# Kernel optimization log

Hardware: AMD Instinct MI355X
Metric: run time of the kernel (lower is better)

The kernel has to match this reference:

```python
import jax, jax.numpy as jnp
import numpy as np

N_NODES = 50000
N_EDGES = 800000
D_IN = 64
F1 = 64
F2 = 64
D_HID = 100


def setup_inputs() -> dict:
    key = jax.random.key(0)
    ks = jax.random.split(key, 12)
    x = jax.random.normal(ks[0], (N_NODES, D_IN), dtype=jnp.float32)
    edge_src = jax.random.randint(ks[1], (N_EDGES,), 0, N_NODES, dtype=jnp.int32)
    edge_dst = jax.random.randint(ks[2], (N_EDGES,), 0, N_NODES, dtype=jnp.int32)
    # stands in for pre-normalized GCN adjacency values (D^-1/2 (A+I) D^-1/2)
    edge_weight = jax.random.uniform(ks[3], (N_EDGES,), dtype=jnp.float32)
    def glorot(k, shape):
        lim = np.sqrt(6.0 / (shape[0] + shape[1]))
        return jax.random.uniform(k, shape, jnp.float32, -lim, lim)
    W1 = glorot(ks[4], (D_IN, F1))
    b1 = jnp.zeros((F1,), jnp.float32)
    W2 = glorot(ks[5], (F1, F2))
    b2 = jnp.zeros((F2,), jnp.float32)
    Wd = glorot(ks[6], (F2, D_HID))
    bd = jnp.zeros((D_HID,), jnp.float32)
    Wo = glorot(ks[7], (D_HID, 1))
    bo = jnp.zeros((1,), jnp.float32)
    return {"x": x, "edge_src": edge_src, "edge_dst": edge_dst,
            "edge_weight": edge_weight, "W1": W1, "b1": b1, "W2": W2,
            "b2": b2, "Wd": Wd, "bd": bd, "Wo": Wo, "bo": bo}


def _gcn_conv(x, edge_src, edge_dst, edge_weight, W, b):
    # spektral GCNConv: out = swish(A_norm @ (X @ W) + b)
    h = x @ W                                        # [N, F]
    msg = h[edge_src] * edge_weight[:, None]          # [E, F] gather + scale
    agg = jax.ops.segment_sum(msg, edge_dst, num_segments=N_NODES)  # [N, F]
    return jax.nn.swish(agg + b)


def reference(x, edge_src, edge_dst, edge_weight, W1, b1, W2, b2, Wd, bd, Wo, bo):
    h = _gcn_conv(x, edge_src, edge_dst, edge_weight, W1, b1)
    h = _gcn_conv(h, edge_src, edge_dst, edge_weight, W2, b2)
    h = jax.nn.swish(h @ Wd + bd)                    # Dense(100, swish)
    return jax.nn.sigmoid(h @ Wo + bo)               # Dense(1, sigmoid) -> [N, 1]
```

## Files before the change

kernel.cpp:

```cpp
#include <hip/hip_runtime.h>
#include <hip/hip_fp16.h>

#define N_NODES 50000
#define N_EDGES 800000
#define D 64
#define DHID 100
#define NTILES (N_NODES / 16)
#define NCT 7
#define CAP 64
#define NGROUPS 4
#define NSLICES 780
#define FILL_BLOCKS (NGROUPS * NSLICES)
#define MM_BLOCKS ((NTILES + 3) / 4)
#define DST_PER_GROUP (N_NODES / NGROUPS)
#define FSTRIDE (NSLICES * 256)
#define KMAX 5

typedef unsigned short ushort;
typedef unsigned int uint;
typedef __attribute__((ext_vector_type(8))) short s16x8;
typedef __attribute__((ext_vector_type(4))) float f32x4;

#define MFMA16(A, B, C) __builtin_amdgcn_mfma_f32_16x16x32_bf16((A), (B), (C), 0, 0, 0)

__device__ __forceinline__ float swishf(float x) { return x / (1.0f + __expf(-x)); }

__device__ __forceinline__ ushort f2bf(float f) {
    uint u = __float_as_uint(f);
    uint r = (u + 0x7fffu + ((u >> 16) & 1u)) >> 16;
    return (ushort)r;
}
__device__ __forceinline__ float bf2f(ushort h) { return __uint_as_float((uint)h << 16); }
__device__ __forceinline__ float bf_lo(uint d) { return __uint_as_float(d << 16); }
__device__ __forceinline__ float bf_hi(uint d) { return __uint_as_float(d & 0xffff0000u); }

__device__ __forceinline__ float hwf(uint e) {
    return __half2float(__ushort_as_half((ushort)(e >> 16)));
}

__device__ __forceinline__ void accum8(float* acc, uint4 v, float w) {
    acc[0] = fmaf(w, bf_lo(v.x), acc[0]);
    acc[1] = fmaf(w, bf_hi(v.x), acc[1]);
    acc[2] = fmaf(w, bf_lo(v.y), acc[2]);
    acc[3] = fmaf(w, bf_hi(v.y), acc[3]);
    acc[4] = fmaf(w, bf_lo(v.z), acc[4]);
    acc[5] = fmaf(w, bf_hi(v.z), acc[5]);
    acc[6] = fmaf(w, bf_lo(v.w), acc[6]);
    acc[7] = fmaf(w, bf_hi(v.w), acc[7]);
}

__device__ __forceinline__ void gather_node2(const ushort* __restrict__ H,
                                             const uint* __restrict__ bucket,
                                             const int* __restrict__ degp,
                                             int j, int fg, float* acc) {
#pragma unroll
    for (int t = 0; t < 8; ++t) acc[t] = 0.f;
    const int sA = j * 4, sB = 16 + j * 4;
    uint4 eA = *((const uint4*)(bucket + sA));
    uint4 eB = *((const uint4*)(bucket + sB));
    int degv = min(*degp, CAP);

    bool pA = sA < degv, pB = sB < degv;
    uint4 vA0, vA1, vA2, vA3, vB0, vB1, vB2, vB3;
    float wA0 = 0, wA1 = 0, wA2 = 0, wA3 = 0;
    float wB0 = 0, wB1 = 0, wB2 = 0, wB3 = 0;
    if (pA) {
        wA0 = hwf(eA.x);
        wA1 = (sA + 1 < degv) ? hwf(eA.y) : 0.f;
        wA2 = (sA + 2 < degv) ? hwf(eA.z) : 0.f;
        wA3 = (sA + 3 < degv) ? hwf(eA.w) : 0.f;
        uint i0 = min(eA.x & 0xffffu, (uint)(N_NODES - 1));
        uint i1 = min(eA.y & 0xffffu, (uint)(N_NODES - 1));
        uint i2 = min(eA.z & 0xffffu, (uint)(N_NODES - 1));
        uint i3 = min(eA.w & 0xffffu, (uint)(N_NODES - 1));
        vA0 = *((const uint4*)(H + ((size_t)i0 << 6) + (fg << 3)));
        vA1 = *((const uint4*)(H + ((size_t)i1 << 6) + (fg << 3)));
        vA2 = *((const uint4*)(H + ((size_t)i2 << 6) + (fg << 3)));
        vA3 = *((const uint4*)(H + ((size_t)i3 << 6) + (fg << 3)));
    }
    if (pB) {
        wB0 = hwf(eB.x);
        wB1 = (sB + 1 < degv) ? hwf(eB.y) : 0.f;
        wB2 = (sB + 2 < degv) ? hwf(eB.z) : 0.f;
        wB3 = (sB + 3 < degv) ? hwf(eB.w) : 0.f;
        uint i0 = min(eB.x & 0xffffu, (uint)(N_NODES - 1));
        uint i1 = min(eB.y & 0xffffu, (uint)(N_NODES - 1));
        uint i2 = min(eB.z & 0xffffu, (uint)(N_NODES - 1));
        uint i3 = min(eB.w & 0xffffu, (uint)(N_NODES - 1));
        vB0 = *((const uint4*)(H + ((size_t)i0 << 6) + (fg << 3)));
        vB1 = *((const uint4*)(H + ((size_t)i1 << 6) + (fg << 3)));
        vB2 = *((const uint4*)(H + ((size_t)i2 << 6) + (fg << 3)));
        vB3 = *((const uint4*)(H + ((size_t)i3 << 6) + (fg << 3)));
    }
    if (pA) {
        accum8(acc, vA0, wA0);
        accum8(acc, vA1, wA1);
        accum8(acc, vA2, wA2);
        accum8(acc, vA3, wA3);
    }
    if (pB) {
        accum8(acc, vB0, wB0);
        accum8(acc, vB1, wB1);
        accum8(acc, vB2, wB2);
        accum8(acc, vB3, wB3);
    }
    for (int base = 32; base < degv; base += 16) {
        int s0 = base + j * 4;
        if (s0 < degv) {
            uint4 e = *((const uint4*)(bucket + s0));
            float w0 = hwf(e.x);
            float w1 = (s0 + 1 < degv) ? hwf(e.y) : 0.f;
            float w2 = (s0 + 2 < degv) ? hwf(e.z) : 0.f;
            float w3 = (s0 + 3 < degv) ? hwf(e.w) : 0.f;
            uint s0i = min(e.x & 0xffffu, (uint)(N_NODES - 1));
            uint s1i = min(e.y & 0xffffu, (uint)(N_NODES - 1));
            uint s2i = min(e.z & 0xffffu, (uint)(N_NODES - 1));
            uint s3i = min(e.w & 0xffffu, (uint)(N_NODES - 1));
            uint4 v0 = *((const uint4*)(H + ((size_t)s0i << 6) + (fg << 3)));
            uint4 v1 = *((const uint4*)(H + ((size_t)s1i << 6) + (fg << 3)));
            uint4 v2 = *((const uint4*)(H + ((size_t)s2i << 6) + (fg << 3)));
            uint4 v3 = *((const uint4*)(H + ((size_t)s3i << 6) + (fg << 3)));
            accum8(acc, v0, w0);
            accum8(acc, v1, w1);
            accum8(acc, v2, w2);
            accum8(acc, v3, w3);
        }
    }
#pragma unroll
    for (int t = 0; t < 8; ++t) {
        acc[t] += __shfl_xor(acc[t], 8, 64);
        acc[t] += __shfl_xor(acc[t], 16, 64);
    }
}

__global__ __launch_bounds__(256) void fill_and_l1(const int* __restrict__ src,
                                                   const int* __restrict__ dst,
                                                   const float* __restrict__ w,
                                                   int* __restrict__ deg,
                                                   uint* __restrict__ csr,
                                                   const float* __restrict__ X,
                                                   const float* __restrict__ W,
                                                   const float* __restrict__ W2,
                                                   const float* __restrict__ Wd,
                                                   short* __restrict__ W2T2,
                                                   short* __restrict__ WdT2,
                                                   ushort* __restrict__ H) {
    __shared__ __align__(16) short sBT[2][D][72];
    int tid = threadIdx.x;

    if (blockIdx.x < FILL_BLOCKS) {
        const int g = blockIdx.x & (NGROUPS - 1);
        const int s = blockIdx.x >> 2;
        const int lo = g * DST_PER_GROUP;
        const int e0 = s * 256 + tid;
        int d[KMAX];
        bool mk[KMAX];
#pragma unroll
        for (int k = 0; k < KMAX; ++k) {
            int e = e0 + k * FSTRIDE;
            int dv = (e < N_EDGES) ? dst[e] : -1;
            d[k] = dv;
            mk[k] = ((uint)(dv - lo) < (uint)DST_PER_GROUP);
        }
        float wv5[KMAX];
        int sv5[KMAX];
#pragma unroll
        for (int k = 0; k < KMAX; ++k)
            if (mk[k]) {
                int e = e0 + k * FSTRIDE;
                wv5[k] = w[e];
                sv5[k] = src[e];
            }
        int r5[KMAX];
#pragma unroll
        for (int k = 0; k < KMAX; ++k)
            if (mk[k]) r5[k] = atomicAdd(&deg[d[k]], 1);
#pragma unroll
        for (int k = 0; k < KMAX; ++k)
            if (mk[k]) {
                uint hw = (uint)__half_as_ushort(__float2half_rn(wv5[k]));
                uint payload = (uint)sv5[k] | (hw << 16);
                int r = min(r5[k], CAP - 1);
                csr[(d[k] << 6) + r] = payload;
            }
        return;
    }

    if (blockIdx.x >= FILL_BLOCKS + MM_BLOCKS) {
        if (blockIdx.x == FILL_BLOCKS + MM_BLOCKS) {
            for (int idx = tid; idx < D * D; idx += 256) {
                int k = idx >> 6, c = idx & 63;
                float wv = W2[idx];
                ushort hi = f2bf(wv);
                W2T2[(size_t)c * D + k] = (short)hi;
                W2T2[(size_t)(D + c) * D + k] = (short)f2bf(wv - bf2f(hi));
            }
        } else {
            for (int idx = tid; idx < NCT * 16 * D; idx += 256) {
                int jj = idx >> 6, k = idx & 63;
                float wv = (jj < DHID) ? Wd[k * DHID + jj] : 0.f;
                ushort hi = f2bf(wv);
                WdT2[(size_t)jj * D + k] = (short)hi;
                WdT2[(size_t)(NCT * 16 + jj) * D + k] = (short)f2bf(wv - bf2f(hi));
            }
        }
        return;
    }

    for (int idx = tid; idx < D * D; idx += 256) {
        int k = idx >> 6, c = idx & 63;
        float wv = W[idx];
        ushort hi = f2bf(wv);
        sBT[0][c][k] = (short)hi;
        sBT[1][c][k] = (short)f2bf(wv - bf2f(hi));
    }
    __syncthreads();
    int wv_ = tid >> 6, lane = tid & 63, quad = lane >> 4, m = lane & 15;
    int tile = min((blockIdx.x - FILL_BLOCKS) * 4 + wv_, NTILES - 1);
    int node0 = tile * 16;

    f32x4 acc[4] = {{0,0,0,0},{0,0,0,0},{0,0,0,0},{0,0,0,0}};
#pragma unroll
    for (int kt = 0; kt < 2; ++kt) {
        int k0 = kt * 32 + quad * 8;
        const float* xp = X + ((size_t)(node0 + m) << 6) + k0;
        float4 xa = *((const float4*)xp);
        float4 xb = *((const float4*)(xp + 4));
        float xv[8] = {xa.x, xa.y, xa.z, xa.w, xb.x, xb.y, xb.z, xb.w};
        s16x8 ahi, alo;
#pragma unroll
        for (int jj = 0; jj < 8; ++jj) {
            ushort hi = f2bf(xv[jj]);
            ahi[jj] = (short)hi;
            alo[jj] = (short)f2bf(xv[jj] - bf2f(hi));
        }
#pragma unroll
        for (int ct = 0; ct < 4; ++ct) {
            int n = ct * 16 + m;
            s16x8 bhi = *((const s16x8*)&sBT[0][n][k0]);
            s16x8 blo = *((const s16x8*)&sBT[1][n][k0]);
            acc[ct] = MFMA16(ahi, bhi, acc[ct]);
            acc[ct] = MFMA16(ahi, blo, acc[ct]);
            acc[ct] = MFMA16(alo, bhi, acc[ct]);
        }
    }
    __syncthreads();
    short (*rep)[16][72] = (short(*)[16][72])&sBT[0][0][0];
#pragma unroll
    for (int ct = 0; ct < 4; ++ct)
#pragma unroll
        for (int r = 0; r < 4; ++r)
            rep[wv_][quad * 4 + r][ct * 16 + m] = (short)f2bf(acc[ct][r]);
#pragma unroll
    for (int half = 0; half < 2; ++half) {
        int r = (lane >> 3) + half * 8;
        int c0 = (lane & 7) * 8;
        s16x8 v = *((const s16x8*)&rep[wv_][r][c0]);
        *((s16x8*)(H + ((size_t)(node0 + r) << 6) + c0)) = v;
    }
}

__global__ __launch_bounds__(256) void gather_act(const ushort* __restrict__ H,
                                                  const int* __restrict__ deg,
                                                  const uint* __restrict__ csr,
                                                  const float* __restrict__ bias,
                                                  ushort* __restrict__ actOut) {
    int tid = threadIdx.x;
    int wave = tid >> 6, lane = tid & 63;
    int h = lane >> 5, j = (lane >> 3) & 3, fg = lane & 7;
    int node = blockIdx.x * 8 + wave * 2 + h;
    const uint* bucket = csr + ((size_t)node << 6);

    float acc[8];
    gather_node2(H, bucket, deg + node, j, fg, acc);
    if (j == 0) {
        float4 ba = ((const float4*)bias)[fg * 2];
        float4 bb = ((const float4*)bias)[fg * 2 + 1];
        float r0 = swishf(acc[0] + ba.x);
        float r1 = swishf(acc[1] + ba.y);
        float r2 = swishf(acc[2] + ba.z);
        float r3 = swishf(acc[3] + ba.w);
        float r4 = swishf(acc[4] + bb.x);
        float r5 = swishf(acc[5] + bb.y);
        float r6 = swishf(acc[6] + bb.z);
        float r7 = swishf(acc[7] + bb.w);
        uint4 u;
        u.x = (uint)f2bf(r0) | ((uint)f2bf(r1) << 16);
        u.y = (uint)f2bf(r2) | ((uint)f2bf(r3) << 16);
        u.z = (uint)f2bf(r4) | ((uint)f2bf(r5) << 16);
        u.w = (uint)f2bf(r6) | ((uint)f2bf(r7) << 16);
        *((uint4*)(actOut + ((size_t)node << 6) + (fg << 3))) = u;
    }
}

__global__ __launch_bounds__(256) void gather_tail(const ushort* __restrict__ act1,
                                                   const int* __restrict__ deg,
                                                   const uint* __restrict__ csr,
                                                   const short* __restrict__ W2T2,
                                                   const float* __restrict__ b2,
                                                   const short* __restrict__ WdT2,
                                                   const float* __restrict__ bd,
                                                   const float* __restrict__ Wo,
                                                   const float* __restrict__ bo,
                                                   float* __restrict__ out) {
    __shared__ __align__(16) float sAgg[16][72];
    __shared__ __align__(16) short sAct2[16][72];
    __shared__ float sPart[4][16];
    int tid = threadIdx.x;
    int wv = tid >> 6, lane = tid & 63;
    int h = lane >> 5, j = (lane >> 3) & 3, fg = lane & 7;
    int quad = lane >> 4, m = lane & 15;
    int node0 = blockIdx.x * 16;

    for (int t = 0; t < 2; ++t) {
        int nl = wv * 4 + t * 2 + h;
        int node = node0 + nl;
        const uint* bucket = csr + ((size_t)node << 6);
        float acc[8];
        gather_node2(act1, bucket, deg + node, j, fg, acc);
        if (j == 0) {
            float4 u0 = {acc[0], acc[1], acc[2], acc[3]};
            float4 u1 = {acc[4], acc[5], acc[6], acc[7]};
            *((float4*)&sAgg[nl][fg * 8]) = u0;
            *((float4*)&sAgg[nl][fg * 8 + 4]) = u1;
        }
    }
    __syncthreads();

    {
        f32x4 acc = {0, 0, 0, 0};
        int n = wv * 16 + m;
#pragma unroll
        for (int kt = 0; kt < 2; ++kt) {
            int k0 = kt * 32 + quad * 8;
            float4 xa = *((const float4*)&sAgg[m][k0]);
            float4 xb = *((const float4*)&sAgg[m][k0 + 4]);
            float xv[8] = {xa.x, xa.y, xa.z, xa.w, xb.x, xb.y, xb.z, xb.w};
            s16x8 ahi, alo;
#pragma unroll
            for (int jj = 0; jj < 8; ++jj) {
                ushort hi = f2bf(xv[jj]);
                ahi[jj] = (short)hi;
                alo[jj] = (short)f2bf(xv[jj] - bf2f(hi));
            }
            s16x8 bhi = *((const s16x8*)(W2T2 + (size_t)n * D + k0));
            s16x8 blo = *((const s16x8*)(W2T2 + (size_t)(D + n) * D + k0));
            acc = MFMA16(ahi, bhi, acc);
            acc = MFMA16(ahi, blo, acc);
            acc = MFMA16(alo, bhi, acc);
        }
        float bv = b2[n];
#pragma unroll
        for (int r = 0; r < 4; ++r)
            sAct2[quad * 4 + r][n] = (short)f2bf(swishf(acc[r] + bv));
    }
    __syncthreads();

    float part[4] = {0, 0, 0, 0};
#pragma unroll
    for (int cc = 0; cc < 2; ++cc) {
        int ct = wv + cc * 4;
        if (ct < NCT) {
            f32x4 acc = {0, 0, 0, 0};
            int n = ct * 16 + m;
#pragma unroll
            for (int kt = 0; kt < 2; ++kt) {
                int k0 = kt * 32 + quad * 8;
                s16x8 a = *((const s16x8*)&sAct2[m][k0]);
                s16x8 bhi = *((const s16x8*)(WdT2 + (size_t)n * D + k0));
                s16x8 blo = *((const s16x8*)(WdT2 + (size_t)(NCT * 16 + n) * D + k0));
                acc = MFMA16(a, bhi, acc);
                acc = MFMA16(a, blo, acc);
            }
            float bdv = (n < DHID) ? bd[n] : 0.f;
            float wov = (n < DHID) ? Wo[n] : 0.f;
#pragma unroll
            for (int r = 0; r < 4; ++r)
                part[r] = fmaf(swishf(acc[r] + bdv), wov, part[r]);
        }
    }
#pragma unroll
    for (int r = 0; r < 4; ++r) {
        part[r] += __shfl_xor(part[r], 1, 64);
        part[r] += __shfl_xor(part[r], 2, 64);
        part[r] += __shfl_xor(part[r], 4, 64);
        part[r] += __shfl_xor(part[r], 8, 64);
    }
    if (m == 0) {
#pragma unroll
        for (int r = 0; r < 4; ++r)
            sPart[wv][quad * 4 + r] = part[r];
    }
    __syncthreads();
    if (tid < 16) {
        float z = sPart[0][tid] + sPart[1][tid] + sPart[2][tid] + sPart[3][tid] + bo[0];
        out[blockIdx.x * 16 + tid] = 1.f / (1.f + __expf(-z));
    }
}

extern "C" void kernel_launch(void* const* d_in, const int* in_sizes, int n_in,
                              void* d_out, int out_size, void* d_ws, size_t ws_size,
                              hipStream_t stream) {
    const float* x   = (const float*)d_in[0];
    const int* esrc  = (const int*)d_in[1];
    const int* edst  = (const int*)d_in[2];
    const float* ew  = (const float*)d_in[3];
    const float* W1  = (const float*)d_in[4];
    const float* b1  = (const float*)d_in[5];
    const float* W2  = (const float*)d_in[6];
    const float* b2  = (const float*)d_in[7];
    const float* Wd  = (const float*)d_in[8];
    const float* bd  = (const float*)d_in[9];
    const float* Wo  = (const float*)d_in[10];
    const float* bo  = (const float*)d_in[11];
    float* out = (float*)d_out;

    char* ws = (char*)d_ws;
    ushort* H1   = (ushort*)ws;  ws += (size_t)N_NODES * D * sizeof(ushort);
    ushort* act1 = (ushort*)ws;  ws += (size_t)N_NODES * D * sizeof(ushort);
    uint* csr    = (uint*)ws;    ws += (size_t)N_NODES * CAP * sizeof(uint);
    int* deg     = (int*)ws;     ws += (size_t)N_NODES * sizeof(int);
    short* W2T2  = (short*)ws;   ws += (size_t)2 * D * D * sizeof(short);
    short* WdT2  = (short*)ws;   ws += (size_t)2 * NCT * 16 * D * sizeof(short);

    const int gBlocks = N_NODES / 8;

    hipMemsetAsync(deg, 0, (size_t)N_NODES * sizeof(int), stream);

    fill_and_l1<<<FILL_BLOCKS + MM_BLOCKS + 2, 256, 0, stream>>>(
        esrc, edst, ew, deg, csr, x, W1, W2, Wd, W2T2, WdT2, H1);

    gather_act<<<gBlocks, 256, 0, stream>>>(H1, deg, csr, b1, act1);

    gather_tail<<<NTILES, 256, 0, stream>>>(act1, deg, csr, W2T2, b2, WdT2, bd, Wo, bo, out);
}
```

Measured before the change: 182.1 us.

## Split per-node CSR buckets into two halves with separate degree counters

Each destination node's 64-slot bucket is split into two 32-slot halves, and fill blocks pick a half by slice parity. Each half has its own atomic degree counter, which halves contention on the degree atomics, and the gather reads both counters with one int2 load. The gather loop is rewritten as fixed unrolled passes over the two halves. Edge weight, source and X loads are made nontemporal. The trade-off is that a node overflows if more than 32 of its edges land in one half, which is tighter than the old single cap of 64.

```diff
diff --git a/kernel.cpp b/kernel.cpp
--- a/kernel.cpp
+++ b/kernel.cpp
@@ -55,20 +55,21 @@
                                              int j, int fg, float* acc) {
 #pragma unroll
     for (int t = 0; t < 8; ++t) acc[t] = 0.f;
-    const int sA = j * 4, sB = 16 + j * 4;
-    uint4 eA = *((const uint4*)(bucket + sA));
-    uint4 eB = *((const uint4*)(bucket + sB));
-    int degv = min(*degp, CAP);
-
-    bool pA = sA < degv, pB = sB < degv;
+    const int sj = j * 4;
+    uint4 eA = *((const uint4*)(bucket + sj));
+    uint4 eB = *((const uint4*)(bucket + 32 + sj));
+    int2 dd = *((const int2*)degp);
+    int dA = min(dd.x, 32), dB = min(dd.y, 32);
+
+    bool pA = sj < dA, pB = sj < dB;
     uint4 vA0, vA1, vA2, vA3, vB0, vB1, vB2, vB3;
     float wA0 = 0, wA1 = 0, wA2 = 0, wA3 = 0;
     float wB0 = 0, wB1 = 0, wB2 = 0, wB3 = 0;
     if (pA) {
         wA0 = hwf(eA.x);
-        wA1 = (sA + 1 < degv) ? hwf(eA.y) : 0.f;
-        wA2 = (sA + 2 < degv) ? hwf(eA.z) : 0.f;
-        wA3 = (sA + 3 < degv) ? hwf(eA.w) : 0.f;
+        wA1 = (sj + 1 < dA) ? hwf(eA.y) : 0.f;
+        wA2 = (sj + 2 < dA) ? hwf(eA.z) : 0.f;
+        wA3 = (sj + 3 < dA) ? hwf(eA.w) : 0.f;
         uint i0 = min(eA.x & 0xffffu, (uint)(N_NODES - 1));
         uint i1 = min(eA.y & 0xffffu, (uint)(N_NODES - 1));
         uint i2 = min(eA.z & 0xffffu, (uint)(N_NODES - 1));
@@ -80,9 +81,9 @@
     }
     if (pB) {
         wB0 = hwf(eB.x);
-        wB1 = (sB + 1 < degv) ? hwf(eB.y) : 0.f;
-        wB2 = (sB + 2 < degv) ? hwf(eB.z) : 0.f;
-        wB3 = (sB + 3 < degv) ? hwf(eB.w) : 0.f;
+        wB1 = (sj + 1 < dB) ? hwf(eB.y) : 0.f;
+        wB2 = (sj + 2 < dB) ? hwf(eB.z) : 0.f;
+        wB3 = (sj + 3 < dB) ? hwf(eB.w) : 0.f;
         uint i0 = min(eB.x & 0xffffu, (uint)(N_NODES - 1));
         uint i1 = min(eB.y & 0xffffu, (uint)(N_NODES - 1));
         uint i2 = min(eB.z & 0xffffu, (uint)(N_NODES - 1));
@@ -104,28 +105,50 @@
         accum8(acc, vB2, wB2);
         accum8(acc, vB3, wB3);
     }
-    for (int base = 32; base < degv; base += 16) {
-        int s0 = base + j * 4;
-        if (s0 < degv) {
+    if (dA > 16) {
+        int s0 = 16 + sj;
+        if (s0 < dA) {
             uint4 e = *((const uint4*)(bucket + s0));
             float w0 = hwf(e.x);
-            float w1 = (s0 + 1 < degv) ? hwf(e.y) : 0.f;
-            float w2 = (s0 + 2 < degv) ? hwf(e.z) : 0.f;
-            float w3 = (s0 + 3 < degv) ? hwf(e.w) : 0.f;
-            uint s0i = min(e.x & 0xffffu, (uint)(N_NODES - 1));
-            uint s1i = min(e.y & 0xffffu, (uint)(N_NODES - 1));
-            uint s2i = min(e.z & 0xffffu, (uint)(N_NODES - 1));
-            uint s3i = min(e.w & 0xffffu, (uint)(N_NODES - 1));
-            uint4 v0 = *((const uint4*)(H + ((size_t)s0i << 6) + (fg << 3)));
-            uint4 v1 = *((const uint4*)(H + ((size_t)s1i << 6) + (fg << 3)));
-            uint4 v2 = *((const uint4*)(H + ((size_t)s2i << 6) + (fg << 3)));
-            uint4 v3 = *((const uint4*)(H + ((size_t)s3i << 6) + (fg << 3)));
+            float w1 = (s0 + 1 < dA) ? hwf(e.y) : 0.f;
+            float w2 = (s0 + 2 < dA) ? hwf(e.z) : 0.f;
+            float w3 = (s0 + 3 < dA) ? hwf(e.w) : 0.f;
+            uint i0 = min(e.x & 0xffffu, (uint)(N_NODES - 1));
+            uint i1 = min(e.y & 0xffffu, (uint)(N_NODES - 1));
+            uint i2 = min(e.z & 0xffffu, (uint)(N_NODES - 1));
+            uint i3 = min(e.w & 0xffffu, (uint)(N_NODES - 1));
+            uint4 v0 = *((const uint4*)(H + ((size_t)i0 << 6) + (fg << 3)));
+            uint4 v1 = *((const uint4*)(H + ((size_t)i1 << 6) + (fg << 3)));
+            uint4 v2 = *((const uint4*)(H + ((size_t)i2 << 6) + (fg << 3)));
+            uint4 v3 = *((const uint4*)(H + ((size_t)i3 << 6) + (fg << 3)));
             accum8(acc, v0, w0);
             accum8(acc, v1, w1);
             accum8(acc, v2, w2);
             accum8(acc, v3, w3);
         }
     }
+    if (dB > 16) {
+        int s0 = 16 + sj;
+        if (s0 < dB) {
+            uint4 e = *((const uint4*)(bucket + 32 + s0));
+            float w0 = hwf(e.x);
+            float w1 = (s0 + 1 < dB) ? hwf(e.y) : 0.f;
+            float w2 = (s0 + 2 < dB) ? hwf(e.z) : 0.f;
+            float w3 = (s0 + 3 < dB) ? hwf(e.w) : 0.f;
+            uint i0 = min(e.x & 0xffffu, (uint)(N_NODES - 1));
+            uint i1 = min(e.y & 0xffffu, (uint)(N_NODES - 1));
+            uint i2 = min(e.z & 0xffffu, (uint)(N_NODES - 1));
+            uint i3 = min(e.w & 0xffffu, (uint)(N_NODES - 1));
+            uint4 v0 = *((const uint4*)(H + ((size_t)i0 << 6) + (fg << 3)));
+            uint4 v1 = *((const uint4*)(H + ((size_t)i1 << 6) + (fg << 3)));
+            uint4 v2 = *((const uint4*)(H + ((size_t)i2 << 6) + (fg << 3)));
+            uint4 v3 = *((const uint4*)(H + ((size_t)i3 << 6) + (fg << 3)));
+            accum8(acc, v0, w0);
+            accum8(acc, v1, w1);
+            accum8(acc, v2, w2);
+            accum8(acc, v3, w3);
+        }
+    }
 #pragma unroll
     for (int t = 0; t < 8; ++t) {
         acc[t] += __shfl_xor(acc[t], 8, 64);
@@ -136,7 +159,7 @@
 __global__ __launch_bounds__(256) void fill_and_l1(const int* __restrict__ src,
                                                    const int* __restrict__ dst,
                                                    const float* __restrict__ w,
-                                                   int* __restrict__ deg,
+                                                   int* __restrict__ deg2,
                                                    uint* __restrict__ csr,
                                                    const float* __restrict__ X,
                                                    const float* __restrict__ W,
@@ -151,6 +174,7 @@
     if (blockIdx.x < FILL_BLOCKS) {
         const int g = blockIdx.x & (NGROUPS - 1);
         const int s = blockIdx.x >> 2;
+        const int p = s & 1;
         const int lo = g * DST_PER_GROUP;
         const int e0 = s * 256 + tid;
         int d[KMAX];
@@ -168,20 +192,20 @@
         for (int k = 0; k < KMAX; ++k)
             if (mk[k]) {
                 int e = e0 + k * FSTRIDE;
-                wv5[k] = w[e];
-                sv5[k] = src[e];
+                wv5[k] = __builtin_nontemporal_load(w + e);
+                sv5[k] = __builtin_nontemporal_load(src + e);
             }
         int r5[KMAX];
 #pragma unroll
         for (int k = 0; k < KMAX; ++k)
-            if (mk[k]) r5[k] = atomicAdd(&deg[d[k]], 1);
+            if (mk[k]) r5[k] = atomicAdd(&deg2[(d[k] << 1) + p], 1);
 #pragma unroll
         for (int k = 0; k < KMAX; ++k)
             if (mk[k]) {
                 uint hw = (uint)__half_as_ushort(__float2half_rn(wv5[k]));
                 uint payload = (uint)sv5[k] | (hw << 16);
-                int r = min(r5[k], CAP - 1);
-                csr[(d[k] << 6) + r] = payload;
+                int r = min(r5[k], 31);
+                csr[(d[k] << 6) + (p << 5) + r] = payload;
             }
         return;
     }
@@ -224,9 +248,9 @@
     for (int kt = 0; kt < 2; ++kt) {
         int k0 = kt * 32 + quad * 8;
         const float* xp = X + ((size_t)(node0 + m) << 6) + k0;
-        float4 xa = *((const float4*)xp);
-        float4 xb = *((const float4*)(xp + 4));
-        float xv[8] = {xa.x, xa.y, xa.z, xa.w, xb.x, xb.y, xb.z, xb.w};
+        f32x4 xa = __builtin_nontemporal_load((const f32x4*)xp);
+        f32x4 xb = __builtin_nontemporal_load((const f32x4*)(xp + 4));
+        float xv[8] = {xa[0], xa[1], xa[2], xa[3], xb[0], xb[1], xb[2], xb[3]};
         s16x8 ahi, alo;
 #pragma unroll
         for (int jj = 0; jj < 8; ++jj) {
@@ -261,7 +285,7 @@
 }
 
 __global__ __launch_bounds__(256) void gather_act(const ushort* __restrict__ H,
-                                                  const int* __restrict__ deg,
+                                                  const int* __restrict__ deg2,
                                                   const uint* __restrict__ csr,
                                                   const float* __restrict__ bias,
                                                   ushort* __restrict__ actOut) {
@@ -272,7 +296,7 @@
     const uint* bucket = csr + ((size_t)node << 6);
 
     float acc[8];
-    gather_node2(H, bucket, deg + node, j, fg, acc);
+    gather_node2(H, bucket, deg2 + (node << 1), j, fg, acc);
     if (j == 0) {
         float4 ba = ((const float4*)bias)[fg * 2];
         float4 bb = ((const float4*)bias)[fg * 2 + 1];
@@ -294,7 +318,7 @@
 }
 
 __global__ __launch_bounds__(256) void gather_tail(const ushort* __restrict__ act1,
-                                                   const int* __restrict__ deg,
+                                                   const int* __restrict__ deg2,
                                                    const uint* __restrict__ csr,
                                                    const short* __restrict__ W2T2,
                                                    const float* __restrict__ b2,
@@ -317,7 +341,7 @@
         int node = node0 + nl;
         const uint* bucket = csr + ((size_t)node << 6);
         float acc[8];
-        gather_node2(act1, bucket, deg + node, j, fg, acc);
+        gather_node2(act1, bucket, deg2 + (node << 1), j, fg, acc);
         if (j == 0) {
             float4 u0 = {acc[0], acc[1], acc[2], acc[3]};
             float4 u1 = {acc[4], acc[5], acc[6], acc[7]};
@@ -394,7 +418,7 @@
     __syncthreads();
     if (tid < 16) {
         float z = sPart[0][tid] + sPart[1][tid] + sPart[2][tid] + sPart[3][tid] + bo[0];
-        out[blockIdx.x * 16 + tid] = 1.f / (1.f + __expf(-z));
+        out[node0 + tid] = 1.f / (1.f + __expf(-z));
     }
 }
 
@@ -419,18 +443,18 @@
     ushort* H1   = (ushort*)ws;  ws += (size_t)N_NODES * D * sizeof(ushort);
     ushort* act1 = (ushort*)ws;  ws += (size_t)N_NODES * D * sizeof(ushort);
     uint* csr    = (uint*)ws;    ws += (size_t)N_NODES * CAP * sizeof(uint);
-    int* deg     = (int*)ws;     ws += (size_t)N_NODES * sizeof(int);
+    int* deg2    = (int*)ws;     ws += (size_t)2 * N_NODES * sizeof(int);
     short* W2T2  = (short*)ws;   ws += (size_t)2 * D * D * sizeof(short);
     short* WdT2  = (short*)ws;   ws += (size_t)2 * NCT * 16 * D * sizeof(short);
 
     const int gBlocks = N_NODES / 8;
 
-    hipMemsetAsync(deg, 0, (size_t)N_NODES * sizeof(int), stream);
+    hipMemsetAsync(deg2, 0, (size_t)2 * N_NODES * sizeof(int), stream);
 
     fill_and_l1<<<FILL_BLOCKS + MM_BLOCKS + 2, 256, 0, stream>>>(
-        esrc, edst, ew, deg, csr, x, W1, W2, Wd, W2T2, WdT2, H1);
-
-    gather_act<<<gBlocks, 256, 0, stream>>>(H1, deg, csr, b1, act1);
-
-    gather_tail<<<NTILES, 256, 0, stream>>>(act1, deg, csr, W2T2, b2, WdT2, bd, Wo, bo, out);
-}
+        esrc, edst, ew, deg2, csr, x, W1, W2, Wd, W2T2, WdT2, H1);
+
+    gather_act<<<gBlocks, 256, 0, stream>>>(H1, deg2, csr, b1, act1);
+
+    gather_tail<<<NTILES, 256, 0, stream>>>(act1, deg2, csr, W2T2, b2, WdT2, bd, Wo, bo, out);
+}
```

Measured after the change: 186.4 us. 1.02x slower.

## Persistent grid-stride gather with prefetched CSR buckets and nontemporal streaming loads

Applied to the files above, without the earlier changes.

gather_act becomes a persistent kernel of 1024 blocks that walks node pairs with a grid stride and prefetches the next pair's CSR entries and degree while the current pair is gathered. gather_tail issues both nodes' bucket and degree loads up front so their latency overlaps. Streaming reads of edge weights, sources and x in the fill kernel now use nontemporal loads to spare the cache. The aim is to hide index-load latency, at the cost of lower occupancy and a looped tail in the persistent kernel.

```diff
diff --git a/kernel.cpp b/kernel.cpp
--- a/kernel.cpp
+++ b/kernel.cpp
@@ -15,6 +15,7 @@
 #define DST_PER_GROUP (N_NODES / NGROUPS)
 #define FSTRIDE (NSLICES * 256)
 #define KMAX 5
+#define GA_BLOCKS 1024
 
 typedef unsigned short ushort;
 typedef unsigned int uint;
@@ -49,17 +50,13 @@
     acc[7] = fmaf(w, bf_hi(v.w), acc[7]);
 }
 
-__device__ __forceinline__ void gather_node2(const ushort* __restrict__ H,
-                                             const uint* __restrict__ bucket,
-                                             const int* __restrict__ degp,
-                                             int j, int fg, float* acc) {
+__device__ __forceinline__ void gather_body(const ushort* __restrict__ H,
+                                            const uint* __restrict__ bucket,
+                                            uint4 eA, uint4 eB, int degv,
+                                            int j, int fg, float* acc) {
 #pragma unroll
     for (int t = 0; t < 8; ++t) acc[t] = 0.f;
     const int sA = j * 4, sB = 16 + j * 4;
-    uint4 eA = *((const uint4*)(bucket + sA));
-    uint4 eB = *((const uint4*)(bucket + sB));
-    int degv = min(*degp, CAP);
-
     bool pA = sA < degv, pB = sB < degv;
     uint4 vA0, vA1, vA2, vA3, vB0, vB1, vB2, vB3;
     float wA0 = 0, wA1 = 0, wA2 = 0, wA3 = 0;
@@ -168,8 +165,8 @@
         for (int k = 0; k < KMAX; ++k)
             if (mk[k]) {
                 int e = e0 + k * FSTRIDE;
-                wv5[k] = w[e];
-                sv5[k] = src[e];
+                wv5[k] = __builtin_nontemporal_load(w + e);
+                sv5[k] = __builtin_nontemporal_load(src + e);
             }
         int r5[KMAX];
 #pragma unroll
@@ -224,9 +221,9 @@
     for (int kt = 0; kt < 2; ++kt) {
         int k0 = kt * 32 + quad * 8;
         const float* xp = X + ((size_t)(node0 + m) << 6) + k0;
-        float4 xa = *((const float4*)xp);
-        float4 xb = *((const float4*)(xp + 4));
-        float xv[8] = {xa.x, xa.y, xa.z, xa.w, xb.x, xb.y, xb.z, xb.w};
+        f32x4 xa = __builtin_nontemporal_load((const f32x4*)xp);
+        f32x4 xb = __builtin_nontemporal_load((const f32x4*)(xp + 4));
+        float xv[8] = {xa[0], xa[1], xa[2], xa[3], xb[0], xb[1], xb[2], xb[3]};
         s16x8 ahi, alo;
 #pragma unroll
         for (int jj = 0; jj < 8; ++jj) {
@@ -268,28 +265,50 @@
     int tid = threadIdx.x;
     int wave = tid >> 6, lane = tid & 63;
     int h = lane >> 5, j = (lane >> 3) & 3, fg = lane & 7;
-    int node = blockIdx.x * 8 + wave * 2 + h;
+    const int NPAIRS = N_NODES / 2;
+    const int stride = GA_BLOCKS * 4;
+    int pair = blockIdx.x * 4 + wave;
+    if (pair >= NPAIRS) return;
+
+    int node = pair * 2 + h;
     const uint* bucket = csr + ((size_t)node << 6);
-
-    float acc[8];
-    gather_node2(H, bucket, deg + node, j, fg, acc);
-    if (j == 0) {
-        float4 ba = ((const float4*)bias)[fg * 2];
-        float4 bb = ((const float4*)bias)[fg * 2 + 1];
-        float r0 = swishf(acc[0] + ba.x);
-        float r1 = swishf(acc[1] + ba.y);
-        float r2 = swishf(acc[2] + ba.z);
-        float r3 = swishf(acc[3] + ba.w);
-        float r4 = swishf(acc[4] + bb.x);
-        float r5 = swishf(acc[5] + bb.y);
-        float r6 = swishf(acc[6] + bb.z);
-        float r7 = swishf(acc[7] + bb.w);
-        uint4 u;
-        u.x = (uint)f2bf(r0) | ((uint)f2bf(r1) << 16);
-        u.y = (uint)f2bf(r2) | ((uint)f2bf(r3) << 16);
-        u.z = (uint)f2bf(r4) | ((uint)f2bf(r5) << 16);
-        u.w = (uint)f2bf(r6) | ((uint)f2bf(r7) << 16);
-        *((uint4*)(actOut + ((size_t)node << 6) + (fg << 3))) = u;
+    uint4 eA = *((const uint4*)(bucket + j * 4));
+    uint4 eB = *((const uint4*)(bucket + 16 + j * 4));
+    int degv = min(deg[node], CAP);
+
+    for (;;) {
+        int npair = pair + stride;
+        bool more = (npair < NPAIRS);
+        int nnode = more ? (npair * 2 + h) : node;
+        const uint* nbucket = csr + ((size_t)nnode << 6);
+        uint4 neA = *((const uint4*)(nbucket + j * 4));
+        uint4 neB = *((const uint4*)(nbucket + 16 + j * 4));
+        int ndeg = min(deg[nnode], CAP);
+
+        float acc[8];
+        gather_body(H, bucket, eA, eB, degv, j, fg, acc);
+        if (j == 0) {
+            float4 ba = ((const float4*)bias)[fg * 2];
+            float4 bb = ((const float4*)bias)[fg * 2 + 1];
+            float r0 = swishf(acc[0] + ba.x);
+            float r1 = swishf(acc[1] + ba.y);
+            float r2 = swishf(acc[2] + ba.z);
+            float r3 = swishf(acc[3] + ba.w);
+            float r4 = swishf(acc[4] + bb.x);
+            float r5 = swishf(acc[5] + bb.y);
+            float r6 = swishf(acc[6] + bb.z);
+            float r7 = swishf(acc[7] + bb.w);
+            uint4 u;
+            u.x = (uint)f2bf(r0) | ((uint)f2bf(r1) << 16);
+            u.y = (uint)f2bf(r2) | ((uint)f2bf(r3) << 16);
+            u.z = (uint)f2bf(r4) | ((uint)f2bf(r5) << 16);
+            u.w = (uint)f2bf(r6) | ((uint)f2bf(r7) << 16);
+            *((uint4*)(actOut + ((size_t)node << 6) + (fg << 3))) = u;
+        }
+
+        if (!more) break;
+        pair = npair; node = nnode; bucket = nbucket;
+        eA = neA; eB = neB; degv = ndeg;
     }
 }
 
@@ -312,17 +331,33 @@
     int quad = lane >> 4, m = lane & 15;
     int node0 = blockIdx.x * 16;
 
-    for (int t = 0; t < 2; ++t) {
-        int nl = wv * 4 + t * 2 + h;
-        int node = node0 + nl;
-        const uint* bucket = csr + ((size_t)node << 6);
-        float acc[8];
-        gather_node2(act1, bucket, deg + node, j, fg, acc);
+    {
+        int n0l = wv * 4 + h, n1l = wv * 4 + 2 + h;
+        int n0 = node0 + n0l, n1 = node0 + n1l;
+        const uint* b0 = csr + ((size_t)n0 << 6);
+        const uint* b1 = csr + ((size_t)n1 << 6);
+        uint4 eA0 = *((const uint4*)(b0 + j * 4));
+        uint4 eB0 = *((const uint4*)(b0 + 16 + j * 4));
+        uint4 eA1 = *((const uint4*)(b1 + j * 4));
+        uint4 eB1 = *((const uint4*)(b1 + 16 + j * 4));
+        int d0 = min(deg[n0], CAP);
+        int d1 = min(deg[n1], CAP);
+
+        float acc0[8];
+        gather_body(act1, b0, eA0, eB0, d0, j, fg, acc0);
         if (j == 0) {
-            float4 u0 = {acc[0], acc[1], acc[2], acc[3]};
-            float4 u1 = {acc[4], acc[5], acc[6], acc[7]};
-            *((float4*)&sAgg[nl][fg * 8]) = u0;
-            *((float4*)&sAgg[nl][fg * 8 + 4]) = u1;
+            float4 u0 = {acc0[0], acc0[1], acc0[2], acc0[3]};
+            float4 u1 = {acc0[4], acc0[5], acc0[6], acc0[7]};
+            *((float4*)&sAgg[n0l][fg * 8]) = u0;
+            *((float4*)&sAgg[n0l][fg * 8 + 4]) = u1;
+        }
+        float acc1[8];
+        gather_body(act1, b1, eA1, eB1, d1, j, fg, acc1);
+        if (j == 0) {
+            float4 u0 = {acc1[0], acc1[1], acc1[2], acc1[3]};
+            float4 u1 = {acc1[4], acc1[5], acc1[6], acc1[7]};
+            *((float4*)&sAgg[n1l][fg * 8]) = u0;
+            *((float4*)&sAgg[n1l][fg * 8 + 4]) = u1;
         }
     }
     __syncthreads();
@@ -394,7 +429,7 @@
     __syncthreads();
     if (tid < 16) {
         float z = sPart[0][tid] + sPart[1][tid] + sPart[2][tid] + sPart[3][tid] + bo[0];
-        out[blockIdx.x * 16 + tid] = 1.f / (1.f + __expf(-z));
+        out[node0 + tid] = 1.f / (1.f + __expf(-z));
     }
 }
 
@@ -423,14 +458,12 @@
     short* W2T2  = (short*)ws;   ws += (size_t)2 * D * D * sizeof(short);
     short* WdT2  = (short*)ws;   ws += (size_t)2 * NCT * 16 * D * sizeof(short);
 
-    const int gBlocks = N_NODES / 8;
-
     hipMemsetAsync(deg, 0, (size_t)N_NODES * sizeof(int), stream);
 
     fill_and_l1<<<FILL_BLOCKS + MM_BLOCKS + 2, 256, 0, stream>>>(
         esrc, edst, ew, deg, csr, x, W1, W2, Wd, W2T2, WdT2, H1);
 
-    gather_act<<<gBlocks, 256, 0, stream>>>(H1, deg, csr, b1, act1);
+    gather_act<<<GA_BLOCKS, 256, 0, stream>>>(H1, deg, csr, b1, act1);
 
     gather_tail<<<NTILES, 256, 0, stream>>>(act1, deg, csr, W2T2, b2, WdT2, bd, Wo, bo, out);
 }
```

Result: no change. 185.5 us (+1.9%).
